# Kernel tuning notes

Hardware: AMD Instinct MI355X
Metric: run time of the kernel (lower is better)

The kernel has to match this reference:

```python
import jax, jax.numpy as jnp
import numpy as np

N_NODES = 50000
N_EDGES = 600000
D_IN = 128
HID = 128
N_LAYERS = 4
N_OUT = 8
BN_EPS = 1e-5


def setup_inputs() -> dict:
    key = jax.random.key(0)
    ks = jax.random.split(key, 12)
    x = jax.random.normal(ks[0], (N_NODES, D_IN), dtype=jnp.float32)
    edge_index = jax.random.randint(ks[1], (2, N_EDGES), 0, N_NODES, dtype=jnp.int64)
    s = 1.0 / np.sqrt(HID)
    # per-layer GIN MLP params, stacked over layers (d_in == hidden so shapes match)
    W1 = jax.random.uniform(ks[2], (N_LAYERS, HID, HID), jnp.float32, -s, s)
    b1 = jax.random.uniform(ks[3], (N_LAYERS, HID), jnp.float32, -s, s)
    W2 = jax.random.uniform(ks[4], (N_LAYERS, HID, HID), jnp.float32, -s, s)
    b2 = jax.random.uniform(ks[5], (N_LAYERS, HID), jnp.float32, -s, s)
    gamma = jnp.ones((N_LAYERS, HID), jnp.float32)
    beta = jnp.zeros((N_LAYERS, HID), jnp.float32)
    s1 = 1.0 / np.sqrt(N_LAYERS * HID)
    lin1_W = jax.random.uniform(ks[6], (N_LAYERS * HID, HID), jnp.float32, -s1, s1)
    lin1_b = jax.random.uniform(ks[7], (HID,), jnp.float32, -s1, s1)
    lin2_W = jax.random.uniform(ks[8], (HID, N_OUT), jnp.float32, -s, s)
    lin2_b = jax.random.uniform(ks[9], (N_OUT,), jnp.float32, -s, s)
    return dict(x=x, edge_index=edge_index, W1=W1, b1=b1, W2=W2, b2=b2,
                gamma=gamma, beta=beta, lin1_W=lin1_W, lin1_b=lin1_b,
                lin2_W=lin2_W, lin2_b=lin2_b)


def _gin_layer(x, src, dst, W1, b1, W2, b2, g, bt):
    # GINConv, eps=0: h_i = MLP(x_i + sum_{j in N(i)} x_j)
    agg = jax.ops.segment_sum(x[src], dst, num_segments=N_NODES)  # [N, d]
    h = x + agg
    h = jax.nn.relu(h @ W1 + b1)
    h = jax.nn.relu(h @ W2 + b2)
    # BatchNorm1d (training-mode stats, biased variance)
    mean = jnp.mean(h, axis=0)
    var = jnp.var(h, axis=0)
    return (h - mean) * jax.lax.rsqrt(var + BN_EPS) * g + bt


def reference(x, edge_index, W1, b1, W2, b2, gamma, beta,
              lin1_W, lin1_b, lin2_W, lin2_b):
    src, dst = edge_index[0], edge_index[1]
    xs = []
    h = x
    for l in range(N_LAYERS):
        h = _gin_layer(h, src, dst, W1[l], b1[l], W2[l], b2[l], gamma[l], beta[l])
        xs.append(h)
    jk = jnp.concatenate(xs, axis=-1)          # JumpingKnowledge 'cat' -> [N, L*HID]
    out = jax.nn.relu(jk @ lin1_W + lin1_b)    # dropout is identity at inference
    out = out @ lin2_W + lin2_b                # [N, N_OUT]
    return out
```

## Files before the change

kernel.cpp:

```cpp
#include <hip/hip_runtime.h>

#define NNODES 50000
#define NEDGES 600000
#define HID 128
#define NLAYERS 4
#define NOUT 8
#define BN_EPS 1e-5f
#define NBLK 196
#define NPBLK 3125
#define NCOPY 8
#define IDXCAP 1024

typedef short short8 __attribute__((ext_vector_type(8)));
typedef float f32x4 __attribute__((ext_vector_type(4)));

__device__ inline unsigned short f2bf(float f) {
  unsigned u = __float_as_uint(f);
  unsigned r = ((u >> 16) & 1u) + 0x7fffu;
  return (unsigned short)((u + r) >> 16);
}
__device__ inline float bflo(unsigned w) { return __uint_as_float(w << 16); }
__device__ inline float bfhi(unsigned w) { return __uint_as_float(w & 0xffff0000u); }


__global__ void detect64_k(const int* __restrict__ ei, int* __restrict__ flag) {
  __shared__ int anynz;
  if (threadIdx.x == 0) anynz = 0;
  __syncthreads();
  int acc = 0;
  for (int i = threadIdx.x; i < 4096; i += 256) {
    int p = i * 146;
    acc |= ei[2 * p + 1];
  }
  if (acc != 0) anynz = 1;
  __syncthreads();
  if (threadIdx.x == 0) *flag = (anynz == 0) ? 1 : 0;
}

__global__ void cvt_bf_k(const float* __restrict__ src, unsigned short* __restrict__ dst,
                         int n4) {
  int i = blockIdx.x * 256 + threadIdx.x;
  if (i >= n4) return;
  float4 v = ((const float4*)src)[i];
  ushort4 o;
  o.x = f2bf(v.x);
  o.y = f2bf(v.y);
  o.z = f2bf(v.z);
  o.w = f2bf(v.w);
  ((ushort4*)dst)[i] = o;
}


__global__ void zero_degc_k(int* __restrict__ degC) {
  int i = blockIdx.x * 256 + threadIdx.x;
  if (i < NCOPY * NNODES) degC[i] = 0;
}

__global__ void hist_rank_k(const int* __restrict__ ei, const int* __restrict__ flag,
                            int* __restrict__ degC, int* __restrict__ rank) {
  int e = blockIdx.x * 256 + threadIdx.x;
  if (e >= NEDGES) return;
  int d = (*flag) ? ei[2 * NEDGES + 2 * e] : ei[NEDGES + e];
  int c = blockIdx.x & (NCOPY - 1);
  rank[e] = atomicAdd(&degC[c * NNODES + d], 1);
}

__global__ void coff_k(int* __restrict__ degC, int* __restrict__ deg) {
  int d = blockIdx.x * 256 + threadIdx.x;
  if (d >= NNODES) return;
  int run = 0;
#pragma unroll
  for (int c = 0; c < NCOPY; ++c) {
    int t = degC[c * NNODES + d];
    degC[c * NNODES + d] = run;
    run += t;
  }
  deg[d] = run;
}

__global__ void blocksum_k(const int* __restrict__ deg, int* __restrict__ bsum) {
  int t = threadIdx.x;
  int i = blockIdx.x * 256 + t;
  __shared__ int sh[256];
  sh[t] = (i < NNODES) ? deg[i] : 0;
  __syncthreads();
  for (int s = 128; s > 0; s >>= 1) {
    if (t < s) sh[t] += sh[t + s];
    __syncthreads();
  }
  if (t == 0) bsum[blockIdx.x] = sh[0];
}

__global__ void scanb_k(const int* __restrict__ bsum, int* __restrict__ boff) {
  __shared__ int sh[256];
  int t = threadIdx.x;
  sh[t] = (t < NBLK) ? bsum[t] : 0;
  __syncthreads();
  for (int d = 1; d < 256; d <<= 1) {
    int v = (t >= d) ? sh[t - d] : 0;
    __syncthreads();
    sh[t] += v;
    __syncthreads();
  }
  if (t < NBLK) boff[t] = (t == 0) ? 0 : sh[t - 1];
}

__global__ void writeoff_k(const int* __restrict__ deg, const int* __restrict__ boff,
                           int* __restrict__ off) {
  int t = threadIdx.x;
  int i = blockIdx.x * 256 + t;
  __shared__ int sh[256];
  int v = (i < NNODES) ? deg[i] : 0;
  sh[t] = v;
  __syncthreads();
  for (int d = 1; d < 256; d <<= 1) {
    int u = (t >= d) ? sh[t - d] : 0;
    __syncthreads();
    sh[t] += u;
    __syncthreads();
  }
  int excl = boff[blockIdx.x] + sh[t] - v;
  if (i < NNODES) off[i] = excl;
  if (i == NNODES - 1) off[NNODES] = excl + v;
}

__global__ void fill2_k(const int* __restrict__ ei, const int* __restrict__ flag,
                        const int* __restrict__ off, const int* __restrict__ degC,
                        const int* __restrict__ rank, int* __restrict__ srcs) {
  int e = blockIdx.x * 256 + threadIdx.x;
  if (e >= NEDGES) return;
  int s, d;
  if (*flag) {
    s = ei[2 * e];
    d = ei[2 * NEDGES + 2 * e];
  } else {
    s = ei[e];
    d = ei[NEDGES + e];
  }
  int c = blockIdx.x & (NCOPY - 1);
  srcs[off[d] + degC[c * NNODES + d] + rank[e]] = s;
}

__global__ void gather_agg_k(const unsigned short* __restrict__ X,
                             const int* __restrict__ off, const int* __restrict__ srcs,
                             unsigned short* __restrict__ T) {
  __shared__ int sOff[9];
  __shared__ int sIdx[IDXCAP];
  int tid = threadIdx.x;
  int nb = blockIdx.x * 8;
  if (tid < 9) sOff[tid] = off[nb + tid];
  __syncthreads();
  int base = sOff[0];
  int total = sOff[8] - base;
  int stage = total > IDXCAP ? IDXCAP : total;
  for (int t = tid; t < stage; t += 256) sIdx[t] = srcs[base + t];
  __syncthreads();

  int g = tid >> 5, lane = tid & 31;
  int node = nb + g;
  int a = sOff[g] - base, bnd = sOff[g + 1] - base;
  const uint2* Xv = (const uint2*)X;
  uint2 w = Xv[(size_t)node * 32 + lane];
  float a0 = bflo(w.x), a1 = bfhi(w.x), a2 = bflo(w.y), a3 = bfhi(w.y);

  if (total <= IDXCAP) {
    int e = a;
#pragma unroll
    for (; e + 4 <= bnd; e += 4) {
      int s0 = sIdx[e], s1 = sIdx[e + 1], s2 = sIdx[e + 2], s3 = sIdx[e + 3];
      uint2 v0 = Xv[(size_t)s0 * 32 + lane];
      uint2 v1 = Xv[(size_t)s1 * 32 + lane];
      uint2 v2 = Xv[(size_t)s2 * 32 + lane];
      uint2 v3 = Xv[(size_t)s3 * 32 + lane];
      a0 += bflo(v0.x); a1 += bfhi(v0.x); a2 += bflo(v0.y); a3 += bfhi(v0.y);
      a0 += bflo(v1.x); a1 += bfhi(v1.x); a2 += bflo(v1.y); a3 += bfhi(v1.y);
      a0 += bflo(v2.x); a1 += bfhi(v2.x); a2 += bflo(v2.y); a3 += bfhi(v2.y);
      a0 += bflo(v3.x); a1 += bfhi(v3.x); a2 += bflo(v3.y); a3 += bfhi(v3.y);
    }
    for (; e < bnd; ++e) {
      int s = sIdx[e];
      uint2 v = Xv[(size_t)s * 32 + lane];
      a0 += bflo(v.x); a1 += bfhi(v.x); a2 += bflo(v.y); a3 += bfhi(v.y);
    }
  } else {
    for (int e = a; e < bnd; ++e) {
      int s = srcs[base + e];
      uint2 v = Xv[(size_t)s * 32 + lane];
      a0 += bflo(v.x); a1 += bfhi(v.x); a2 += bflo(v.y); a3 += bfhi(v.y);
    }
  }

  uint2 o;
  o.x = (unsigned)f2bf(a0) | ((unsigned)f2bf(a1) << 16);
  o.y = (unsigned)f2bf(a2) | ((unsigned)f2bf(a3) << 16);
  ((uint2*)T)[(size_t)node * 32 + lane] = o;
}

__global__ void packW_k(const float* __restrict__ W1, const float* __restrict__ W2,
                        const float* __restrict__ L1, unsigned short* __restrict__ P) {
  int t = blockIdx.x * 256 + threadIdx.x;
  if (t >= 48 * 512) return;
  int gk = t >> 9;
  int nt = (t >> 6) & 7;
  int lane = t & 63;
  const float* src;
  int kbase;
  if (gk < 16) {
    src = W1 + (gk >> 2) * 16384;
    kbase = (gk & 3) * 32;
  } else if (gk < 32) {
    src = W2 + ((gk - 16) >> 2) * 16384;
    kbase = ((gk - 16) & 3) * 32;
  } else {
    src = L1;
    kbase = (gk - 32) * 32;
  }
  int n = nt * 16 + (lane & 15);
  int k0 = kbase + (lane >> 4) * 8;
  unsigned short* dst = P + (size_t)t * 8;
#pragma unroll
  for (int j = 0; j < 8; ++j) dst[j] = f2bf(src[(size_t)(k0 + j) * HID + n]);
}

__global__ __launch_bounds__(128) void mlp_k(const unsigned short* __restrict__ A,
                                             const unsigned short* __restrict__ P1,
                                             const float* __restrict__ bias1,
                                             const unsigned short* __restrict__ P2,
                                             const float* __restrict__ bias2,
                                             float* __restrict__ H, int M,
                                             float* __restrict__ pstats) {
  __shared__ unsigned short sA[16 * 136];
  int tid = threadIdx.x;
  int lane = tid & 63, w = tid >> 6;
  int rb = blockIdx.x * 16;
  int r = rb + (lane & 15);
  int hi = lane >> 4, c = lane & 15;
  int koff = hi * 8;
  int ntb = w * 4;

  short8 a_[4];
  const unsigned short* Ar = A + (size_t)r * HID + koff;
#pragma unroll
  for (int ks = 0; ks < 4; ++ks) a_[ks] = *(const short8*)(Ar + ks * 32);

  const short8* Bp1 = (const short8*)P1;
  f32x4 acc[4];
#pragma unroll
  for (int nt = 0; nt < 4; ++nt) acc[nt] = (f32x4){0.f, 0.f, 0.f, 0.f};
  short8 bcur[4], bnxt[4];
#pragma unroll
  for (int nt = 0; nt < 4; ++nt) bcur[nt] = Bp1[(ntb + nt) * 64 + lane];
#pragma unroll
  for (int ks = 0; ks < 4; ++ks) {
    if (ks < 3) {
#pragma unroll
      for (int nt = 0; nt < 4; ++nt) bnxt[nt] = Bp1[(ks + 1) * 512 + (ntb + nt) * 64 + lane];
    }
#pragma unroll
    for (int nt = 0; nt < 4; ++nt)
      acc[nt] = __builtin_amdgcn_mfma_f32_16x16x32_bf16(a_[ks], bcur[nt], acc[nt], 0, 0, 0);
    if (ks < 3) {
#pragma unroll
      for (int nt = 0; nt < 4; ++nt) bcur[nt] = bnxt[nt];
    }
  }
#pragma unroll
  for (int nt = 0; nt < 4; ++nt) {
    int col = (ntb + nt) * 16 + c;
    float b = bias1[col];
#pragma unroll
    for (int rr = 0; rr < 4; ++rr) {
      float v = fmaxf(acc[nt][rr] + b, 0.f);
      sA[(hi * 4 + rr) * 136 + col] = f2bf(v);
    }
  }
  __syncthreads();

#pragma unroll
  for (int nt = 0; nt < 4; ++nt) acc[nt] = (f32x4){0.f, 0.f, 0.f, 0.f};
  const short8* Bp2 = (const short8*)P2;
#pragma unroll
  for (int nt = 0; nt < 4; ++nt) bcur[nt] = Bp2[(ntb + nt) * 64 + lane];
#pragma unroll
  for (int ks = 0; ks < 4; ++ks) {
    short8 af = *(const short8*)&sA[c * 136 + ks * 32 + koff];
    if (ks < 3) {
#pragma unroll
      for (int nt = 0; nt < 4; ++nt) bnxt[nt] = Bp2[(ks + 1) * 512 + (ntb + nt) * 64 + lane];
    }
#pragma unroll
    for (int nt = 0; nt < 4; ++nt)
      acc[nt] = __builtin_amdgcn_mfma_f32_16x16x32_bf16(af, bcur[nt], acc[nt], 0, 0, 0);
    if (ks < 3) {
#pragma unroll
      for (int nt = 0; nt < 4; ++nt) bcur[nt] = bnxt[nt];
    }
  }
  float* dst = pstats + (size_t)blockIdx.x * 256;
#pragma unroll
  for (int nt = 0; nt < 4; ++nt) {
    int col = (ntb + nt) * 16 + c;
    float b = bias2[col];
    float s = 0.f, q = 0.f;
#pragma unroll
    for (int rr = 0; rr < 4; ++rr) {
      int row = rb + hi * 4 + rr;
      float v = fmaxf(acc[nt][rr] + b, 0.f);
      H[(size_t)row * HID + col] = v;
      s += v;
      q += v * v;
    }
    s += __shfl_xor(s, 16, 64);
    q += __shfl_xor(q, 16, 64);
    s += __shfl_xor(s, 32, 64);
    q += __shfl_xor(q, 32, 64);
    if (hi == 0) {
      dst[col] = s;
      dst[128 + col] = q;
    }
  }
}

__global__ void reduce_stats_k(const float* __restrict__ pstats, float* __restrict__ stats) {
  __shared__ float sh[256];
  int j = blockIdx.x;
  int t = threadIdx.x;
  float acc = 0.f;
  for (int b = t; b < NPBLK; b += 256) acc += pstats[(size_t)b * 256 + j];
  sh[t] = acc;
  __syncthreads();
  for (int s = 128; s > 0; s >>= 1) {
    if (t < s) sh[t] += sh[t + s];
    __syncthreads();
  }
  if (t == 0) stats[j] = sh[0];
}

__global__ __launch_bounds__(128) void mjkgemm_k(const unsigned short* __restrict__ H0,
                                                 const unsigned short* __restrict__ H1,
                                                 const unsigned short* __restrict__ H2,
                                                 const unsigned short* __restrict__ H3,
                                                 const unsigned short* __restrict__ P,
                                                 const float* __restrict__ bias,
                                                 float* __restrict__ C, int M) {
  int tid = threadIdx.x;
  int lane = tid & 63, w = tid >> 6;
  int rb = blockIdx.x * 16;
  int r = rb + (lane & 15);
  int koff = (lane >> 4) * 8;
  int ntb = w * 4;
  f32x4 acc[4];
#pragma unroll
  for (int nt = 0; nt < 4; ++nt) acc[nt] = (f32x4){0.f, 0.f, 0.f, 0.f};
  const unsigned short* Hs[4] = {H0, H1, H2, H3};
  short8 bcur[4], bnxt[4];
  for (int l = 0; l < 4; ++l) {
    const short8* Bp = (const short8*)(P + l * 16384);
    short8 a_[4];
    const unsigned short* Ar = Hs[l] + (size_t)r * HID + koff;
#pragma unroll
    for (int ks = 0; ks < 4; ++ks) a_[ks] = *(const short8*)(Ar + ks * 32);
#pragma unroll
    for (int nt = 0; nt < 4; ++nt) bcur[nt] = Bp[(ntb + nt) * 64 + lane];
#pragma unroll
    for (int ks = 0; ks < 4; ++ks) {
      if (ks < 3) {
#pragma unroll
        for (int nt = 0; nt < 4; ++nt) bnxt[nt] = Bp[(ks + 1) * 512 + (ntb + nt) * 64 + lane];
      }
#pragma unroll
      for (int nt = 0; nt < 4; ++nt)
        acc[nt] = __builtin_amdgcn_mfma_f32_16x16x32_bf16(a_[ks], bcur[nt], acc[nt], 0, 0, 0);
      if (ks < 3) {
#pragma unroll
        for (int nt = 0; nt < 4; ++nt) bcur[nt] = bnxt[nt];
      }
    }
  }
  int hi = lane >> 4, c = lane & 15;
#pragma unroll
  for (int nt = 0; nt < 4; ++nt) {
    int col = (ntb + nt) * 16 + c;
    float b = bias[col];
#pragma unroll
    for (int rr = 0; rr < 4; ++rr) {
      int row = rb + hi * 4 + rr;
      float v = fmaxf(acc[nt][rr] + b, 0.f);
      C[(size_t)row * HID + col] = v;
    }
  }
}

__global__ void bn_norm_k(const float* __restrict__ H, unsigned short* __restrict__ HB,
                          const float* __restrict__ stats, const float* __restrict__ gamma,
                          const float* __restrict__ beta) {
  int i = blockIdx.x * 256 + threadIdx.x;
  if (i >= NNODES * 32) return;
  int c4 = i & 31;
  float4 v = ((const float4*)H)[i];
  float4 sm = ((const float4*)stats)[c4];
  float4 sq = ((const float4*)(stats + 128))[c4];
  float4 g = ((const float4*)gamma)[c4];
  float4 bt = ((const float4*)beta)[c4];
  const float invN = 1.0f / (float)NNODES;
  float m, var, inv;
  ushort4 o;
  m = sm.x * invN; var = sq.x * invN - m * m; inv = rsqrtf(var + BN_EPS);
  o.x = f2bf((v.x - m) * inv * g.x + bt.x);
  m = sm.y * invN; var = sq.y * invN - m * m; inv = rsqrtf(var + BN_EPS);
  o.y = f2bf((v.y - m) * inv * g.y + bt.y);
  m = sm.z * invN; var = sq.z * invN - m * m; inv = rsqrtf(var + BN_EPS);
  o.z = f2bf((v.z - m) * inv * g.z + bt.z);
  m = sm.w * invN; var = sq.w * invN - m * m; inv = rsqrtf(var + BN_EPS);
  o.w = f2bf((v.w - m) * inv * g.w + bt.w);
  ((ushort4*)HB)[i] = o;
}

__global__ void head_k(const float* __restrict__ O1, const float* __restrict__ W,
                       const float* __restrict__ b, float* __restrict__ out, int M) {
  __shared__ float sW[HID * NOUT];
  int tid = threadIdx.x;
#pragma unroll
  for (int i = 0; i < 4; ++i) sW[tid + i * 256] = W[tid + i * 256];
  __syncthreads();
  int row = blockIdx.x * 256 + tid;
  if (row >= M) return;
  float acc[NOUT];
#pragma unroll
  for (int j = 0; j < NOUT; ++j) acc[j] = b[j];
  const float* Ar = O1 + (size_t)row * HID;
  for (int k = 0; k < HID; k += 4) {
    float4 a = *(const float4*)(Ar + k);
#pragma unroll
    for (int kk = 0; kk < 4; ++kk) {
      float av = ((const float*)&a)[kk];
#pragma unroll
      for (int j = 0; j < NOUT; ++j) acc[j] += av * sW[(k + kk) * NOUT + j];
    }
  }
#pragma unroll
  for (int j = 0; j < NOUT; ++j) out[(size_t)row * NOUT + j] = acc[j];
}


extern "C" void kernel_launch(void* const* d_in, const int* in_sizes, int n_in,
                              void* d_out, int out_size, void* d_ws, size_t ws_size,
                              hipStream_t stream) {
  const float* x     = (const float*)d_in[0];
  const int*   ei    = (const int*)d_in[1];
  const float* W1    = (const float*)d_in[2];
  const float* b1    = (const float*)d_in[3];
  const float* W2    = (const float*)d_in[4];
  const float* b2    = (const float*)d_in[5];
  const float* gamma = (const float*)d_in[6];
  const float* beta  = (const float*)d_in[7];
  const float* l1W   = (const float*)d_in[8];
  const float* l1b   = (const float*)d_in[9];
  const float* l2W   = (const float*)d_in[10];
  const float* l2b   = (const float*)d_in[11];

  float* ws = (float*)d_ws;
  const size_t NB = (size_t)NNODES * HID;
  const size_t NBH = NB / 2;
  float* h = ws;
  float* t2 = ws + NB;
  unsigned short* xb = (unsigned short*)(ws + 2 * NB);
  unsigned short* tmp = (unsigned short*)(ws + 2 * NB + NBH);
  unsigned short* hb[4];
  for (int l = 0; l < 4; ++l)
    hb[l] = (unsigned short*)(ws + 2 * NB + (2 + l) * NBH);
  float* stats = ws + 2 * NB + 6 * NBH;
  int* flag = (int*)(stats + 1024);
  int* deg = flag + 4;
  int* off = deg + (NNODES + 1);
  int* bsum = off + (NNODES + 1);
  int* boff = bsum + 256;
  int* degC = boff + 260;
  int* rank = degC + NCOPY * NNODES;
  int* srcs = rank + NEDGES;
  size_t pofs = 2 * NB + 6 * NBH + 1024 + 4 + 2 * (size_t)(NNODES + 1) + 256 + 260 +
                (size_t)NCOPY * NNODES + 2 * (size_t)NEDGES;
  pofs = (pofs + 3) & ~(size_t)3;
  unsigned short* P = (unsigned short*)(ws + pofs);
  float* pstats = ws + pofs + 98304;

  detect64_k<<<1, 256, 0, stream>>>(ei, flag);
  zero_degc_k<<<1563, 256, 0, stream>>>(degC);
  hist_rank_k<<<2344, 256, 0, stream>>>(ei, flag, degC, rank);
  coff_k<<<NBLK, 256, 0, stream>>>(degC, deg);
  blocksum_k<<<NBLK, 256, 0, stream>>>(deg, bsum);
  scanb_k<<<1, 256, 0, stream>>>(bsum, boff);
  writeoff_k<<<NBLK, 256, 0, stream>>>(deg, boff, off);
  fill2_k<<<2344, 256, 0, stream>>>(ei, flag, off, degC, rank, srcs);
  packW_k<<<96, 256, 0, stream>>>(W1, W2, l1W, P);
  cvt_bf_k<<<6250, 256, 0, stream>>>(x, xb, NNODES * 32);

  const unsigned short* hin = xb;
  for (int l = 0; l < NLAYERS; ++l) {
    gather_agg_k<<<6250, 256, 0, stream>>>(hin, off, srcs, tmp);
    mlp_k<<<NPBLK, 128, 0, stream>>>(tmp, P + (size_t)l * 16384, b1 + l * HID,
                                     P + 65536 + (size_t)l * 16384, b2 + l * HID, h, NNODES,
                                     pstats);
    reduce_stats_k<<<256, 256, 0, stream>>>(pstats, stats + l * 256);
    bn_norm_k<<<6250, 256, 0, stream>>>(h, hb[l], stats + l * 256, gamma + l * HID,
                                        beta + l * HID);
    hin = hb[l];
  }
  mjkgemm_k<<<NPBLK, 128, 0, stream>>>(hb[0], hb[1], hb[2], hb[3], P + 131072, l1b, t2, NNODES);
  head_k<<<196, 256, 0, stream>>>(t2, l2W, l2b, (float*)d_out, NNODES);
}
```

Measured before the change: 327.9 us.

## Fold BatchNorm affine into next gather and JK weights, drop bn_norm pass

The MLP kernel now stores the pre-BN ReLU output directly as bf16, and BatchNorm becomes a per-column affine (alpha, beta) computed in the stats reduction. That affine is applied inside the next layer's gather, scaled by in-degree plus one, and folded into the packed JK weights and a precomputed JK bias. This removes the separate normalization pass and the fp32 intermediate write/read per layer. In exchange it adds small weight-repacking and bias kernels, a serial single-block bias loop, and it quantizes un-normalized activations to bf16, which may change rounding error.

New measurement: 331.6 us. Within noise of the previous version (+1.1%).

```diff
diff --git a/kernel.cpp b/kernel.cpp
--- a/kernel.cpp
+++ b/kernel.cpp
@@ -141,9 +141,10 @@
   srcs[off[d] + degC[c * NNODES + d] + rank[e]] = s;
 }
 
+template <bool AFFINE>
 __global__ void gather_agg_k(const unsigned short* __restrict__ X,
                              const int* __restrict__ off, const int* __restrict__ srcs,
-                             unsigned short* __restrict__ T) {
+                             const float* __restrict__ ab, unsigned short* __restrict__ T) {
   __shared__ int sOff[9];
   __shared__ int sIdx[IDXCAP];
   int tid = threadIdx.x;
@@ -190,6 +191,16 @@
     }
   }
 
+  if (AFFINE) {
+    float4 al = *(const float4*)(ab + lane * 4);
+    float4 be = *(const float4*)(ab + 128 + lane * 4);
+    float dp1 = (float)(bnd - a + 1);
+    a0 = al.x * a0 + dp1 * be.x;
+    a1 = al.y * a1 + dp1 * be.y;
+    a2 = al.z * a2 + dp1 * be.z;
+    a3 = al.w * a3 + dp1 * be.w;
+  }
+
   uint2 o;
   o.x = (unsigned)f2bf(a0) | ((unsigned)f2bf(a1) << 16);
   o.y = (unsigned)f2bf(a2) | ((unsigned)f2bf(a3) << 16);
@@ -197,9 +208,9 @@
 }
 
 __global__ void packW_k(const float* __restrict__ W1, const float* __restrict__ W2,
-                        const float* __restrict__ L1, unsigned short* __restrict__ P) {
+                        unsigned short* __restrict__ P) {
   int t = blockIdx.x * 256 + threadIdx.x;
-  if (t >= 48 * 512) return;
+  if (t >= 32 * 512) return;
   int gk = t >> 9;
   int nt = (t >> 6) & 7;
   int lane = t & 63;
@@ -208,18 +219,44 @@
   if (gk < 16) {
     src = W1 + (gk >> 2) * 16384;
     kbase = (gk & 3) * 32;
-  } else if (gk < 32) {
+  } else {
     src = W2 + ((gk - 16) >> 2) * 16384;
     kbase = ((gk - 16) & 3) * 32;
-  } else {
-    src = L1;
-    kbase = (gk - 32) * 32;
   }
   int n = nt * 16 + (lane & 15);
   int k0 = kbase + (lane >> 4) * 8;
   unsigned short* dst = P + (size_t)t * 8;
 #pragma unroll
   for (int j = 0; j < 8; ++j) dst[j] = f2bf(src[(size_t)(k0 + j) * HID + n]);
+}
+
+__global__ void packjk_k(const float* __restrict__ L1, const float* __restrict__ ab,
+                         unsigned short* __restrict__ Pjk) {
+  int t = blockIdx.x * 256 + threadIdx.x;
+  if (t >= 16 * 512) return;
+  int gk = t >> 9;
+  int nt = (t >> 6) & 7;
+  int lane = t & 63;
+  int n = nt * 16 + (lane & 15);
+  int k0 = gk * 32 + (lane >> 4) * 8;
+  unsigned short* dst = Pjk + (size_t)t * 8;
+#pragma unroll
+  for (int j = 0; j < 8; ++j) {
+    int K = k0 + j;
+    float al = ab[(K >> 7) * 256 + (K & 127)];
+    dst[j] = f2bf(al * L1[(size_t)K * HID + n]);
+  }
+}
+
+__global__ void biasjk_k(const float* __restrict__ L1, const float* __restrict__ ab,
+                         const float* __restrict__ l1b, float* __restrict__ bjk) {
+  int n = threadIdx.x;
+  float acc = l1b[n];
+  for (int K = 0; K < 4 * HID; ++K) {
+    float be = ab[(K >> 7) * 256 + 128 + (K & 127)];
+    acc += be * L1[(size_t)K * HID + n];
+  }
+  bjk[n] = acc;
 }
 
 __global__ __launch_bounds__(128) void mlp_k(const unsigned short* __restrict__ A,
@@ -227,7 +264,7 @@
                                              const float* __restrict__ bias1,
                                              const unsigned short* __restrict__ P2,
                                              const float* __restrict__ bias2,
-                                             float* __restrict__ H, int M,
+                                             unsigned short* __restrict__ Hq, int M,
                                              float* __restrict__ pstats) {
   __shared__ unsigned short sA[16 * 136];
   int tid = threadIdx.x;
@@ -306,7 +343,7 @@
     for (int rr = 0; rr < 4; ++rr) {
       int row = rb + hi * 4 + rr;
       float v = fmaxf(acc[nt][rr] + b, 0.f);
-      H[(size_t)row * HID + col] = v;
+      Hq[(size_t)row * HID + col] = f2bf(v);
       s += v;
       q += v * v;
     }
@@ -321,19 +358,34 @@
   }
 }
 
-__global__ void reduce_stats_k(const float* __restrict__ pstats, float* __restrict__ stats) {
-  __shared__ float sh[256];
+__global__ void reduce_ab_k(const float* __restrict__ pstats, const float* __restrict__ gamma,
+                            const float* __restrict__ beta, float* __restrict__ ab) {
+  __shared__ float sh[256], sh2[256];
   int j = blockIdx.x;
   int t = threadIdx.x;
-  float acc = 0.f;
-  for (int b = t; b < NPBLK; b += 256) acc += pstats[(size_t)b * 256 + j];
-  sh[t] = acc;
-  __syncthreads();
-  for (int s = 128; s > 0; s >>= 1) {
-    if (t < s) sh[t] += sh[t + s];
+  float s = 0.f, q = 0.f;
+  for (int b = t; b < NPBLK; b += 256) {
+    s += pstats[(size_t)b * 256 + j];
+    q += pstats[(size_t)b * 256 + 128 + j];
+  }
+  sh[t] = s;
+  sh2[t] = q;
+  __syncthreads();
+  for (int st = 128; st > 0; st >>= 1) {
+    if (t < st) {
+      sh[t] += sh[t + st];
+      sh2[t] += sh2[t + st];
+    }
     __syncthreads();
   }
-  if (t == 0) stats[j] = sh[0];
+  if (t == 0) {
+    const float invN = 1.0f / (float)NNODES;
+    float m = sh[0] * invN;
+    float var = sh2[0] * invN - m * m;
+    float al = gamma[j] * rsqrtf(var + BN_EPS);
+    ab[j] = al;
+    ab[128 + j] = beta[j] - m * al;
+  }
 }
 
 __global__ __launch_bounds__(128) void mjkgemm_k(const unsigned short* __restrict__ H0,
@@ -389,31 +441,6 @@
       C[(size_t)row * HID + col] = v;
     }
   }
-}
-
-__global__ void bn_norm_k(const float* __restrict__ H, unsigned short* __restrict__ HB,
-                          const float* __restrict__ stats, const float* __restrict__ gamma,
-                          const float* __restrict__ beta) {
-  int i = blockIdx.x * 256 + threadIdx.x;
-  if (i >= NNODES * 32) return;
-  int c4 = i & 31;
-  float4 v = ((const float4*)H)[i];
-  float4 sm = ((const float4*)stats)[c4];
-  float4 sq = ((const float4*)(stats + 128))[c4];
-  float4 g = ((const float4*)gamma)[c4];
-  float4 bt = ((const float4*)beta)[c4];
-  const float invN = 1.0f / (float)NNODES;
-  float m, var, inv;
-  ushort4 o;
-  m = sm.x * invN; var = sq.x * invN - m * m; inv = rsqrtf(var + BN_EPS);
-  o.x = f2bf((v.x - m) * inv * g.x + bt.x);
-  m = sm.y * invN; var = sq.y * invN - m * m; inv = rsqrtf(var + BN_EPS);
-  o.y = f2bf((v.y - m) * inv * g.y + bt.y);
-  m = sm.z * invN; var = sq.z * invN - m * m; inv = rsqrtf(var + BN_EPS);
-  o.z = f2bf((v.z - m) * inv * g.z + bt.z);
-  m = sm.w * invN; var = sq.w * invN - m * m; inv = rsqrtf(var + BN_EPS);
-  o.w = f2bf((v.w - m) * inv * g.w + bt.w);
-  ((ushort4*)HB)[i] = o;
 }
 
 __global__ void head_k(const float* __restrict__ O1, const float* __restrict__ W,
@@ -462,15 +489,15 @@
   float* ws = (float*)d_ws;
   const size_t NB = (size_t)NNODES * HID;
   const size_t NBH = NB / 2;
-  float* h = ws;
-  float* t2 = ws + NB;
-  unsigned short* xb = (unsigned short*)(ws + 2 * NB);
-  unsigned short* tmp = (unsigned short*)(ws + 2 * NB + NBH);
-  unsigned short* hb[4];
+  float* t2 = ws;
+  unsigned short* xb = (unsigned short*)(ws + NB);
+  unsigned short* tmp = (unsigned short*)(ws + NB + NBH);
+  unsigned short* hq[4];
   for (int l = 0; l < 4; ++l)
-    hb[l] = (unsigned short*)(ws + 2 * NB + (2 + l) * NBH);
-  float* stats = ws + 2 * NB + 6 * NBH;
-  int* flag = (int*)(stats + 1024);
+    hq[l] = (unsigned short*)(ws + NB + (2 + l) * NBH);
+  float* ab = ws + NB + 6 * NBH;
+  float* bjk = ab + 1024;
+  int* flag = (int*)(bjk + 128);
   int* deg = flag + 4;
   int* off = deg + (NNODES + 1);
   int* bsum = off + (NNODES + 1);
@@ -478,10 +505,11 @@
   int* degC = boff + 260;
   int* rank = degC + NCOPY * NNODES;
   int* srcs = rank + NEDGES;
-  size_t pofs = 2 * NB + 6 * NBH + 1024 + 4 + 2 * (size_t)(NNODES + 1) + 256 + 260 +
+  size_t pofs = NB + 6 * NBH + 1024 + 128 + 4 + 2 * (size_t)(NNODES + 1) + 256 + 260 +
                 (size_t)NCOPY * NNODES + 2 * (size_t)NEDGES;
   pofs = (pofs + 3) & ~(size_t)3;
   unsigned short* P = (unsigned short*)(ws + pofs);
+  unsigned short* Pjk = P + 131072;
   float* pstats = ws + pofs + 98304;
 
   detect64_k<<<1, 256, 0, stream>>>(ei, flag);
@@ -492,20 +520,23 @@
   scanb_k<<<1, 256, 0, stream>>>(bsum, boff);
   writeoff_k<<<NBLK, 256, 0, stream>>>(deg, boff, off);
   fill2_k<<<2344, 256, 0, stream>>>(ei, flag, off, degC, rank, srcs);
-  packW_k<<<96, 256, 0, stream>>>(W1, W2, l1W, P);
+  packW_k<<<64, 256, 0, stream>>>(W1, W2, P);
   cvt_bf_k<<<6250, 256, 0, stream>>>(x, xb, NNODES * 32);
 
-  const unsigned short* hin = xb;
   for (int l = 0; l < NLAYERS; ++l) {
-    gather_agg_k<<<6250, 256, 0, stream>>>(hin, off, srcs, tmp);
+    if (l == 0)
+      gather_agg_k<false><<<6250, 256, 0, stream>>>(xb, off, srcs, nullptr, tmp);
+    else
+      gather_agg_k<true><<<6250, 256, 0, stream>>>(hq[l - 1], off, srcs, ab + (l - 1) * 256,
+                                                   tmp);
     mlp_k<<<NPBLK, 128, 0, stream>>>(tmp, P + (size_t)l * 16384, b1 + l * HID,
-                                     P + 65536 + (size_t)l * 16384, b2 + l * HID, h, NNODES,
-                                     pstats);
-    reduce_stats_k<<<256, 256, 0, stream>>>(pstats, stats + l * 256);
-    bn_norm_k<<<6250, 256, 0, stream>>>(h, hb[l], stats + l * 256, gamma + l * HID,
-                                        beta + l * HID);
-    hin = hb[l];
-  }
-  mjkgemm_k<<<NPBLK, 128, 0, stream>>>(hb[0], hb[1], hb[2], hb[3], P + 131072, l1b, t2, NNODES);
+                                     P + 65536 + (size_t)l * 16384, b2 + l * HID, hq[l],
+                                     NNODES, pstats);
+    reduce_ab_k<<<128, 256, 0, stream>>>(pstats, gamma + l * HID, beta + l * HID,
+                                         ab + l * 256);
+  }
+  packjk_k<<<32, 256, 0, stream>>>(l1W, ab, Pjk);
+  biasjk_k<<<1, 128, 0, stream>>>(l1W, ab, l1b, bjk);
+  mjkgemm_k<<<NPBLK, 128, 0, stream>>>(hq[0], hq[1], hq[2], hq[3], Pjk, bjk, t2, NNODES);
   head_k<<<196, 256, 0, stream>>>(t2, l2W, l2b, (float*)d_out, NNODES);
 }
```
